# Performance work log

Measured on AMD Instinct MI355X. Metric: run time of the kernel, lower is better.

Reference implementation:

```python
import jax, jax.numpy as jnp
import numpy as np

N_INST, BATCH, IN_DIM, L_DIM = 256, 128, 1024, 512

def setup_inputs() -> dict:
    key = jax.random.key(0)
    k1, k2, k3, k4 = jax.random.split(key, 4)
    # glorot-uniform-ish scales
    sv = np.sqrt(6.0 / (IN_DIM + L_DIM)).astype(np.float32)
    sw = np.sqrt(6.0 / (L_DIM + 1)).astype(np.float32)
    x = jax.random.normal(k1, (N_INST, BATCH, IN_DIM), dtype=jnp.float32)
    v = jax.random.uniform(k2, (IN_DIM, L_DIM), minval=-sv, maxval=sv, dtype=jnp.float32)
    u = jax.random.uniform(k3, (IN_DIM, L_DIM), minval=-sv, maxval=sv, dtype=jnp.float32)
    w = jax.random.uniform(k4, (L_DIM, 1), minval=-sw, maxval=sw, dtype=jnp.float32)
    return {"x": x, "v": v, "u": u, "w": w}

def reference(x, v, u, w):
    # x: [n_instances, batch, in_dim]
    # Fused batched version of the per-instance loop:
    # score_i = (tanh(x_i @ v) * sigmoid(x_i @ u)) @ w, softmax over instances.
    h = jnp.tanh(jnp.einsum('nbd,dl->nbl', x, v))          # [n, b, l]
    g = jax.nn.sigmoid(jnp.einsum('nbd,dl->nbl', x, u))    # [n, b, l]
    scores = jnp.einsum('nbl,lo->nbo', h * g, w)            # [n, b, 1]
    alpha = jax.nn.softmax(scores, axis=0)                  # softmax over instance axis
    return alpha
```

## Files before the change

kernel.cpp:

```cpp
#include <hip/hip_runtime.h>
#include <stdint.h>

typedef unsigned int  u32;
typedef unsigned short u16;
typedef __bf16 v8bf __attribute__((ext_vector_type(8)));
typedef float  v4f  __attribute__((ext_vector_type(4)));

#define N_INST 256
#define BATCH  128
#define IN_DIM 1024
#define L_DIM  512
#define M_TOT  (N_INST*BATCH)
#define NSLICE 16

#define XB_BYTES   ((size_t)M_TOT * IN_DIM * 2)
#define WPK_BYTES  ((size_t)1024 * IN_DIM * 2)

__device__ inline u32 f2bf_pk(float a, float b){
  u32 ua = __builtin_bit_cast(u32, a);
  u32 ub = __builtin_bit_cast(u32, b);
  ua = (ua + 0x7FFFu + ((ua >> 16) & 1u)) >> 16;
  ub = (ub + 0x7FFFu + ((ub >> 16) & 1u)) & 0xFFFF0000u;
  return ua | ub;
}

__device__ inline void gl2lds16(const u16* g, u16* l){
  __builtin_amdgcn_global_load_lds(
      (const __attribute__((address_space(1))) u32*)(g),
      (__attribute__((address_space(3))) u32*)(l), 16, 0, 0);
}

#define PREP_XBLKS 16384
__global__ void prep(const float* __restrict__ x, const float* __restrict__ v,
                     const float* __restrict__ u, u16* __restrict__ xb,
                     u16* __restrict__ wpk){
  const int b = blockIdx.x;
  if (b < PREP_XBLKS){
    int t = b * 256 + threadIdx.x;
    int r = t >> 6, l = t & 63;
    int kk = r & 1, i = (r >> 1) & 3, h = (r >> 3) & 1, kt = (r >> 4) & 15, mb = r >> 8;
    int q = l >> 4, c = l & 15;
    int row = mb*128 + h*64 + i*16 + c;
    int k0  = kt*64 + kk*32 + q*8;
    const float* src = x + (size_t)row * IN_DIM + k0;
    float4 a0 = *reinterpret_cast<const float4*>(src);
    float4 a1 = *reinterpret_cast<const float4*>(src + 4);
    uint4 out;
    out.x = f2bf_pk(a0.x, a0.y); out.y = f2bf_pk(a0.z, a0.w);
    out.z = f2bf_pk(a1.x, a1.y); out.w = f2bf_pk(a1.z, a1.w);
    *reinterpret_cast<uint4*>(xb + (size_t)r*512 + l*8) = out;
  } else {
    int t = (b - PREP_XBLKS) * 256 + threadIdx.x;
    int r = t >> 6, l = t & 63;
    int kk = r & 1, j = (r >> 1) & 3, kt = (r >> 3) & 15, cs = r >> 7;
    int q = l >> 4, c = l & 15;
    int bcol = cs*4 + j;
    const float* src = (bcol & 1) ? u : v;
    int lcol = (bcol >> 1)*16 + c;
    int k0 = kt*64 + kk*32 + q*8;
    u32 o[4];
#pragma unroll
    for (int ii = 0; ii < 4; ++ii){
      float a  = src[(size_t)(k0 + 2*ii    ) * L_DIM + lcol];
      float bb = src[(size_t)(k0 + 2*ii + 1) * L_DIM + lcol];
      o[ii] = f2bf_pk(a, bb);
    }
    *reinterpret_cast<uint4*>(wpk + (size_t)r*512 + l*8) = make_uint4(o[0], o[1], o[2], o[3]);
  }
}

__launch_bounds__(256, 2)
__global__ void gemm_score(const u16* __restrict__ xb, const u16* __restrict__ wpk,
                           const float* __restrict__ w, float* __restrict__ partial){
  __shared__ __align__(16) u16 Bs[64 * 512];

  const int tid  = threadIdx.x;
  const u32 bid  = blockIdx.x;
  const int xcd  = bid & 7;
  const int slot = bid >> 3;
  const int cs   = slot & 15;
  const int mr   = xcd*8 + (slot >> 4);
  const int mblk0= mr * 4;

  const int lane = tid & 63;
  const int wave = tid >> 6;
  const int q    = lane >> 4;
  const int c    = lane & 15;

  auto stageB = [&](int kh){
    const u16* src = wpk + (size_t)(cs*128 + kh*64) * 512;
#pragma unroll
    for (int it = 0; it < 16; ++it){
      const int rl = wave*16 + it;
      gl2lds16(src + (size_t)rl*512 + lane*8, &Bs[rl*512 + lane*8]);
    }
  };

  const u16* awave = xb + (size_t)mblk0*131072 + (size_t)(2*wave)*1024 + lane*8;

  v4f acc[4][2][4];
#pragma unroll
  for (int mb = 0; mb < 4; ++mb)
#pragma unroll
    for (int gi = 0; gi < 2; ++gi)
#pragma unroll
      for (int j = 0; j < 4; ++j)
        acc[mb][gi][j] = (v4f){0.f, 0.f, 0.f, 0.f};

  stageB(0);
  __syncthreads();

#pragma unroll 1
  for (int kh = 0; kh < 2; ++kh){
#pragma unroll 1
    for (int ktl = 0; ktl < 8; ++ktl){
      const int kt = kh*8 + ktl;
      v8bf bfr[4][2];
#pragma unroll
      for (int j = 0; j < 4; ++j)
#pragma unroll
        for (int kk = 0; kk < 2; ++kk)
          bfr[j][kk] = *reinterpret_cast<const v8bf*>(&Bs[(ktl*8 + j*2 + kk)*512 + lane*8]);
      v8bf af[4][2][2];
      const u16* ak = awave + (size_t)kt * 8192;
#pragma unroll
      for (int mb = 0; mb < 4; ++mb)
#pragma unroll
        for (int gi = 0; gi < 2; ++gi)
#pragma unroll
          for (int kk = 0; kk < 2; ++kk)
            af[mb][gi][kk] = *reinterpret_cast<const v8bf*>(ak + mb*131072 + gi*1024 + kk*512);
#pragma unroll
      for (int mb = 0; mb < 4; ++mb)
#pragma unroll
        for (int kk = 0; kk < 2; ++kk)
#pragma unroll
          for (int gi = 0; gi < 2; ++gi)
#pragma unroll
            for (int j = 0; j < 4; ++j)
              acc[mb][gi][j] = __builtin_amdgcn_mfma_f32_16x16x32_bf16(
                  af[mb][gi][kk], bfr[j][kk], acc[mb][gi][j], 0, 0, 0);
    }
    if (kh == 0){
      __syncthreads();
      stageB(1);
      __syncthreads();
    }
  }

  const float wl0 = w[cs*32 + c];
  const float wl1 = w[cs*32 + 16 + c];
  float* pbase = partial + (size_t)cs * M_TOT;

#pragma unroll
  for (int mb = 0; mb < 4; ++mb){
    float* pout = pbase + (size_t)(mblk0 + mb)*128 + wave*32;
#pragma unroll
    for (int gi = 0; gi < 2; ++gi){
#pragma unroll
      for (int r = 0; r < 4; ++r){
        float t0 = 2.f / (1.f + __expf(-2.f * acc[mb][gi][0][r])) - 1.f;
        float s0 = 1.f / (1.f + __expf(-acc[mb][gi][1][r]));
        float t1 = 2.f / (1.f + __expf(-2.f * acc[mb][gi][2][r])) - 1.f;
        float s1 = 1.f / (1.f + __expf(-acc[mb][gi][3][r]));
        float v2 = t0*s0*wl0 + t1*s1*wl1;
        v2 += __shfl_xor(v2, 1, 64);
        v2 += __shfl_xor(v2, 2, 64);
        v2 += __shfl_xor(v2, 4, 64);
        v2 += __shfl_xor(v2, 8, 64);
        if (c == 0) pout[gi*16 + q*4 + r] = v2;
      }
    }
  }
}

__global__ void softmax_inst(const float* __restrict__ partial, float* __restrict__ out){
  __shared__ float red[N_INST];
  const int b = blockIdx.x;
  const int n = threadIdx.x;
  float s = 0.f;
#pragma unroll
  for (int i = 0; i < NSLICE; ++i) s += partial[(size_t)i * M_TOT + n*BATCH + b];
  red[n] = s; __syncthreads();
  for (int st = N_INST/2; st > 0; st >>= 1){
    if (n < st) red[n] = fmaxf(red[n], red[n + st]);
    __syncthreads();
  }
  float mx = red[0]; __syncthreads();
  float e = __expf(s - mx);
  red[n] = e; __syncthreads();
  for (int st = N_INST/2; st > 0; st >>= 1){
    if (n < st) red[n] += red[n + st];
    __syncthreads();
  }
  out[n*BATCH + b] = e / red[0];
}

extern "C" void kernel_launch(void* const* d_in, const int* in_sizes, int n_in,
                              void* d_out, int out_size, void* d_ws, size_t ws_size,
                              hipStream_t stream) {
  const float* x = (const float*)d_in[0];
  const float* v = (const float*)d_in[1];
  const float* u = (const float*)d_in[2];
  const float* w = (const float*)d_in[3];
  u16*   xb      = (u16*)d_ws;
  u16*   wpk     = (u16*)((char*)d_ws + XB_BYTES);
  float* partial = (float*)((char*)d_ws + XB_BYTES + WPK_BYTES);
  float* out     = (float*)d_out;

  prep<<<dim3(PREP_XBLKS + 512), dim3(256), 0, stream>>>(x, v, u, xb, wpk);
  gemm_score<<<dim3(1024), dim3(256), 0, stream>>>(xb, wpk, w, partial);
  softmax_inst<<<dim3(BATCH), dim3(N_INST), 0, stream>>>(partial, out);
}
```

Baseline: 320.9 us.

## Halve per-block M tile and double-buffer A/B fragment loads in gemm_score

Each block now covers 2 row-blocks instead of 4, with each wave owning 64 rows and all 4 column fragments, and the grid doubles to 2048 blocks. The K loop is unrolled by two with register double buffering, so the next A (global) and B (LDS) fragments load while the current MFMAs run. This targets exposed load latency and adds parallelism. In exchange, each B tile staged into LDS is reused over half as many rows, so total B staging traffic doubles, and register pressure rises.

After: 285.5 us. 11.0% less time.

```diff
diff --git a/kernel.cpp b/kernel.cpp
--- a/kernel.cpp
+++ b/kernel.cpp
@@ -69,6 +69,23 @@
   }
 }
 
+#define LOADA(KT, B_) { const u16* ak_ = awave + (size_t)(KT)*8192;                 \
+  _Pragma("unroll") for (int gi_ = 0; gi_ < 4; ++gi_)                               \
+    _Pragma("unroll") for (int kk_ = 0; kk_ < 2; ++kk_)                             \
+      afb[B_][gi_][kk_] = *reinterpret_cast<const v8bf*>(ak_ + gi_*1024 + kk_*512); }
+
+#define LOADB(KTL, B_) {                                                            \
+  _Pragma("unroll") for (int j_ = 0; j_ < 4; ++j_)                                  \
+    _Pragma("unroll") for (int kk_ = 0; kk_ < 2; ++kk_)                             \
+      bfb[B_][j_][kk_] = *reinterpret_cast<const v8bf*>(&Bs[((KTL)*8 + j_*2 + kk_)*512 + lane*8]); }
+
+#define DOMFMA(B_) {                                                                \
+  _Pragma("unroll") for (int kk_ = 0; kk_ < 2; ++kk_)                               \
+    _Pragma("unroll") for (int gi_ = 0; gi_ < 4; ++gi_)                             \
+      _Pragma("unroll") for (int j_ = 0; j_ < 4; ++j_)                              \
+        acc[gi_][j_] = __builtin_amdgcn_mfma_f32_16x16x32_bf16(                     \
+            afb[B_][gi_][kk_], bfb[B_][j_][kk_], acc[gi_][j_], 0, 0, 0); }
+
 __launch_bounds__(256, 2)
 __global__ void gemm_score(const u16* __restrict__ xb, const u16* __restrict__ wpk,
                            const float* __restrict__ w, float* __restrict__ partial){
@@ -79,8 +96,8 @@
   const int xcd  = bid & 7;
   const int slot = bid >> 3;
   const int cs   = slot & 15;
-  const int mr   = xcd*8 + (slot >> 4);
-  const int mblk0= mr * 4;
+  const int mr   = xcd*16 + (slot >> 4);
+  const int mblk0= mr * 2;
 
   const int lane = tid & 63;
   const int wave = tid >> 6;
@@ -96,80 +113,65 @@
     }
   };
 
-  const u16* awave = xb + (size_t)mblk0*131072 + (size_t)(2*wave)*1024 + lane*8;
-
-  v4f acc[4][2][4];
-#pragma unroll
-  for (int mb = 0; mb < 4; ++mb)
-#pragma unroll
-    for (int gi = 0; gi < 2; ++gi)
-#pragma unroll
-      for (int j = 0; j < 4; ++j)
-        acc[mb][gi][j] = (v4f){0.f, 0.f, 0.f, 0.f};
+  const u16* awave = xb + (size_t)(mblk0 + (wave>>1))*131072
+                        + (size_t)((wave&1)*4)*1024 + lane*8;
+
+  v8bf afb[2][4][2];
+  v8bf bfb[2][4][2];
+  v4f  acc[4][4];
+#pragma unroll
+  for (int gi = 0; gi < 4; ++gi)
+#pragma unroll
+    for (int j = 0; j < 4; ++j)
+      acc[gi][j] = (v4f){0.f, 0.f, 0.f, 0.f};
 
   stageB(0);
+  LOADA(0, 0);
   __syncthreads();
+  LOADB(0, 0);
 
 #pragma unroll 1
-  for (int kh = 0; kh < 2; ++kh){
+  for (int k2 = 0; k2 < 4; ++k2){
+    const int kt = 2*k2;
+    LOADA(kt+1, 1); LOADB(2*k2+1, 1);
+    DOMFMA(0);
+    LOADA(kt+2, 0);
+    if (k2 < 3) LOADB(2*k2+2, 0);
+    DOMFMA(1);
+  }
+  __syncthreads();
+  stageB(1);
+  __syncthreads();
+  LOADB(0, 0);
+
 #pragma unroll 1
-    for (int ktl = 0; ktl < 8; ++ktl){
-      const int kt = kh*8 + ktl;
-      v8bf bfr[4][2];
-#pragma unroll
-      for (int j = 0; j < 4; ++j)
-#pragma unroll
-        for (int kk = 0; kk < 2; ++kk)
-          bfr[j][kk] = *reinterpret_cast<const v8bf*>(&Bs[(ktl*8 + j*2 + kk)*512 + lane*8]);
-      v8bf af[4][2][2];
-      const u16* ak = awave + (size_t)kt * 8192;
-#pragma unroll
-      for (int mb = 0; mb < 4; ++mb)
-#pragma unroll
-        for (int gi = 0; gi < 2; ++gi)
-#pragma unroll
-          for (int kk = 0; kk < 2; ++kk)
-            af[mb][gi][kk] = *reinterpret_cast<const v8bf*>(ak + mb*131072 + gi*1024 + kk*512);
-#pragma unroll
-      for (int mb = 0; mb < 4; ++mb)
-#pragma unroll
-        for (int kk = 0; kk < 2; ++kk)
-#pragma unroll
-          for (int gi = 0; gi < 2; ++gi)
-#pragma unroll
-            for (int j = 0; j < 4; ++j)
-              acc[mb][gi][j] = __builtin_amdgcn_mfma_f32_16x16x32_bf16(
-                  af[mb][gi][kk], bfr[j][kk], acc[mb][gi][j], 0, 0, 0);
-    }
-    if (kh == 0){
-      __syncthreads();
-      stageB(1);
-      __syncthreads();
-    }
+  for (int k2 = 0; k2 < 4; ++k2){
+    const int kt = 8 + 2*k2;
+    LOADA(kt+1, 1); LOADB(2*k2+1, 1);
+    DOMFMA(0);
+    if (k2 < 3){ LOADA(kt+2, 0); LOADB(2*k2+2, 0); }
+    DOMFMA(1);
   }
 
   const float wl0 = w[cs*32 + c];
   const float wl1 = w[cs*32 + 16 + c];
-  float* pbase = partial + (size_t)cs * M_TOT;
-
-#pragma unroll
-  for (int mb = 0; mb < 4; ++mb){
-    float* pout = pbase + (size_t)(mblk0 + mb)*128 + wave*32;
-#pragma unroll
-    for (int gi = 0; gi < 2; ++gi){
-#pragma unroll
-      for (int r = 0; r < 4; ++r){
-        float t0 = 2.f / (1.f + __expf(-2.f * acc[mb][gi][0][r])) - 1.f;
-        float s0 = 1.f / (1.f + __expf(-acc[mb][gi][1][r]));
-        float t1 = 2.f / (1.f + __expf(-2.f * acc[mb][gi][2][r])) - 1.f;
-        float s1 = 1.f / (1.f + __expf(-acc[mb][gi][3][r]));
-        float v2 = t0*s0*wl0 + t1*s1*wl1;
-        v2 += __shfl_xor(v2, 1, 64);
-        v2 += __shfl_xor(v2, 2, 64);
-        v2 += __shfl_xor(v2, 4, 64);
-        v2 += __shfl_xor(v2, 8, 64);
-        if (c == 0) pout[gi*16 + q*4 + r] = v2;
-      }
+  float* pout = partial + (size_t)cs * M_TOT
+              + (size_t)(mblk0 + (wave>>1))*128 + (wave&1)*64;
+
+#pragma unroll
+  for (int gi = 0; gi < 4; ++gi){
+#pragma unroll
+    for (int r = 0; r < 4; ++r){
+      float t0 = 2.f / (1.f + __expf(-2.f * acc[gi][0][r])) - 1.f;
+      float s0 = 1.f / (1.f + __expf(-acc[gi][1][r]));
+      float t1 = 2.f / (1.f + __expf(-2.f * acc[gi][2][r])) - 1.f;
+      float s1 = 1.f / (1.f + __expf(-acc[gi][3][r]));
+      float v2 = t0*s0*wl0 + t1*s1*wl1;
+      v2 += __shfl_xor(v2, 1, 64);
+      v2 += __shfl_xor(v2, 2, 64);
+      v2 += __shfl_xor(v2, 4, 64);
+      v2 += __shfl_xor(v2, 8, 64);
+      if (c == 0) pout[gi*16 + q*4 + r] = v2;
     }
   }
 }
@@ -209,6 +211,6 @@
   float* out     = (float*)d_out;
 
   prep<<<dim3(PREP_XBLKS + 512), dim3(256), 0, stream>>>(x, v, u, xb, wpk);
-  gemm_score<<<dim3(1024), dim3(256), 0, stream>>>(xb, wpk, w, partial);
+  gemm_score<<<dim3(2048), dim3(256), 0, stream>>>(xb, wpk, w, partial);
   softmax_inst<<<dim3(BATCH), dim3(N_INST), 0, stream>>>(partial, out);
 }
```
